# Kernel tuning notes

Hardware: AMD Instinct MI355X
Metric: run time of the kernel (lower is better)

Reference implementation:

```python
import jax, jax.numpy as jnp
import numpy as np

BZ, T, D, DFF, E, BEAMS = 128, 32, 768, 3072, 8, 2


def setup_inputs() -> dict:
    key = jax.random.key(0)
    ks = jax.random.split(key, 4)
    s = 0.02
    return {
        "x": jax.random.normal(ks[0], (BZ, T, D), jnp.float32),
        "attention_mask": jnp.ones((BZ, T), jnp.float32),
        "Wg": jax.random.normal(ks[1], (D, E), jnp.float32) * s,   # gate Linear(D,E,bias=False)
        "W1": jax.random.normal(ks[2], (E, D, DFF), jnp.float32) * s,
        "b1": jnp.zeros((E, DFF), jnp.float32),
        "W2": jax.random.normal(ks[3], (E, DFF, D), jnp.float32) * s,
        "b2": jnp.zeros((E, D), jnp.float32),
    }


def reference(x, attention_mask, Wg, W1, b1, W2, b2):
    # forward_gate: module builds its own all-ones mask regardless of input mask
    mask = jnp.ones((x.shape[0], x.shape[1]), x.dtype)
    x_avg = (x * mask[..., None]).sum(1) / mask[..., None].sum(1)   # [bz, D]
    prob = jax.nn.softmax(x_avg @ Wg, axis=-1)                       # [bz, E]
    # beam_search (layer_judge='first', pre-route): topk on exp(log(softmax)) == softmax probs
    scores = jnp.exp(jnp.log(prob))
    topv, topi = jax.lax.top_k(scores, BEAMS)                        # [bz, beams]
    beam_scores = topv.reshape(-1)                                   # [bz*beams]
    expert_route = topi.reshape(-1, 1)                                # [bz*beams, 1]
    sel = expert_route[:, -1]
    # replicate x per beam: [bz*beams, T, D]
    x_rep = jnp.broadcast_to(x[:, None], (x.shape[0], BEAMS, x.shape[1], x.shape[2]))
    x_rep = x_rep.reshape(-1, x.shape[1], x.shape[2])
    # per-sample expert FFN dispatch (dense masked loop over the E=8 experts)
    out = jnp.zeros_like(x_rep)
    for e in range(E):
        h = jax.nn.gelu(jnp.einsum('nsd,df->nsf', x_rep, W1[e]) + b1[e], approximate=False)
        ye = jnp.einsum('nsf,fd->nsd', h, W2[e]) + b2[e]
        out = jnp.where((sel == e)[:, None, None], ye, out)
    return (out, beam_scores, expert_route)
```

## Files before the change

### kernel.cpp

```cpp
#include <hip/hip_runtime.h>
#include <cstddef>
#include <cstdint>

#define BZd   128
#define Td    32
#define Dd    768
#define DFFd  3072
#define Ed    8
#define NBEAM 256
#define ROWS_TOT 8192
#define OUT_ELEMS 6291456
#define MAXTILES 72

typedef unsigned short u16;
typedef __attribute__((ext_vector_type(4))) unsigned short ushort4v;
typedef __attribute__((ext_vector_type(8))) short frag_ab;
typedef __attribute__((ext_vector_type(4))) float floatx4;

__device__ __forceinline__ u16 f2bf(float f) {
  unsigned int u = __builtin_bit_cast(unsigned int, f);
  u += 0x7FFFu + ((u >> 16) & 1u);
  return (u16)(u >> 16);
}

__device__ __forceinline__ void async_copy16(u16* lds, const u16* g) {
  __builtin_amdgcn_global_load_lds(
      (const __attribute__((address_space(1))) void*)g,
      (__attribute__((address_space(3))) void*)lds, 16, 0, 0);
}

__device__ __forceinline__ float gelu_fast(float x) {
  float z = 1.5957691216f * (x + 0.044715f * x * x * x);
  return x / (1.0f + __expf(-z));
}

__global__ __launch_bounds__(256) void route_kernel(
    const float* __restrict__ x, const float* __restrict__ Wg,
    float* __restrict__ out, int* __restrict__ sel) {
  int b = blockIdx.x;
  int t = threadIdx.x;
  __shared__ float red[256][8];
  float la[8];
#pragma unroll
  for (int e = 0; e < 8; e++) la[e] = 0.f;
  for (int d = t; d < Dd; d += 256) {
    const float* xp = x + (size_t)b * Td * Dd + d;
    float xa = 0.f;
#pragma unroll
    for (int tt = 0; tt < Td; tt++) xa += xp[(size_t)tt * Dd];
    xa *= (1.0f / 32.0f);
#pragma unroll
    for (int e = 0; e < 8; e++) la[e] += xa * Wg[d * 8 + e];
  }
#pragma unroll
  for (int e = 0; e < 8; e++) red[t][e] = la[e];
  __syncthreads();
  for (int s = 128; s > 0; s >>= 1) {
    if (t < s) {
#pragma unroll
      for (int e = 0; e < 8; e++) red[t][e] += red[t + s][e];
    }
    __syncthreads();
  }
  if (t == 0) {
    float lg[8];
#pragma unroll
    for (int e = 0; e < 8; e++) lg[e] = red[0][e];
    float mx = lg[0];
#pragma unroll
    for (int e = 1; e < 8; e++) mx = fmaxf(mx, lg[e]);
    float p[8];
    float sum = 0.f;
#pragma unroll
    for (int e = 0; e < 8; e++) { p[e] = __expf(lg[e] - mx); sum += p[e]; }
    float inv = 1.0f / sum;
#pragma unroll
    for (int e = 0; e < 8; e++) p[e] *= inv;
    int i0 = 0; float v0 = p[0];
#pragma unroll
    for (int e = 1; e < 8; e++) if (p[e] > v0) { v0 = p[e]; i0 = e; }
    int i1 = -1; float v1 = -1.0f;
#pragma unroll
    for (int e = 0; e < 8; e++) if (e != i0 && p[e] > v1) { v1 = p[e]; i1 = e; }
    float* bs = out + OUT_ELEMS;
    float* er = out + OUT_ELEMS + NBEAM;
    bs[2 * b] = v0; bs[2 * b + 1] = v1;
    er[2 * b] = (float)i0; er[2 * b + 1] = (float)i1;
    sel[2 * b] = i0; sel[2 * b + 1] = i1;
  }
}

__global__ __launch_bounds__(256) void bucket_kernel(
    const int* __restrict__ sel, int* __restrict__ perm, int4* __restrict__ tiles) {
  __shared__ int ssel[NBEAM];
  __shared__ int scnt[8];
  __shared__ int soff[8];
  __shared__ int scur[8];
  __shared__ int sperm[NBEAM];
  int t = threadIdx.x;
  ssel[t] = sel[t];
  __syncthreads();
  if (t == 0) {
    for (int e = 0; e < 8; e++) scnt[e] = 0;
    for (int n = 0; n < NBEAM; n++) scnt[ssel[n]]++;
    int o = 0;
    for (int e = 0; e < 8; e++) { soff[e] = o; scur[e] = o; o += scnt[e]; }
    for (int n = 0; n < NBEAM; n++) { int e = ssel[n]; sperm[scur[e]++] = n; }
    int tt = 0;
    for (int e = 0; e < 8; e++) {
      int nr = scnt[e] * 32;
      int base = soff[e] * 32;
      for (int r0 = 0; r0 < nr; r0 += 128) {
        tiles[tt] = make_int4(e, base + r0, min(128, nr - r0), 0);
        tt++;
      }
    }
    for (; tt < MAXTILES; tt++) tiles[tt] = make_int4(-1, 0, 0, 0);
  }
  __syncthreads();
  perm[t] = sperm[t];
}

__global__ __launch_bounds__(256) void convert_x_kernel(
    const float* __restrict__ x, u16* __restrict__ xbf) {
  size_t i = ((size_t)blockIdx.x * 256 + threadIdx.x) * 4;
  float4 v = *(const float4*)(x + i);
  ushort4v pv = {f2bf(v.x), f2bf(v.y), f2bf(v.z), f2bf(v.w)};
  *(ushort4v*)(xbf + i) = pv;
}

__global__ __launch_bounds__(256) void transpose_bf16_kernel(
    const float* __restrict__ in, u16* __restrict__ out, int row0, int col0,
    int ld_in, size_t estr_in, int ld_out, size_t estr_out) {
  __shared__ u16 tile[64][65];
  int e = blockIdx.z;
  int r0 = blockIdx.x * 64, c0 = blockIdx.y * 64;
  int t = threadIdx.x;
  int rr = t >> 4, cc4 = (t & 15) * 4;
  const float* ip = in + (size_t)e * estr_in + (size_t)(row0 + r0) * ld_in + col0 + c0;
#pragma unroll
  for (int i = 0; i < 4; i++) {
    int r = rr + 16 * i;
    float4 v = *(const float4*)(ip + (size_t)r * ld_in + cc4);
    tile[r][cc4 + 0] = f2bf(v.x);
    tile[r][cc4 + 1] = f2bf(v.y);
    tile[r][cc4 + 2] = f2bf(v.z);
    tile[r][cc4 + 3] = f2bf(v.w);
  }
  __syncthreads();
  int ccw = t >> 4, r4 = (t & 15) * 4;
  u16* op = out + (size_t)e * estr_out + (size_t)c0 * ld_out + r0;
#pragma unroll
  for (int i = 0; i < 4; i++) {
    int cc = ccw + 16 * i;
    ushort4v pv = {tile[r4 + 0][cc], tile[r4 + 1][cc], tile[r4 + 2][cc], tile[r4 + 3][cc]};
    *(ushort4v*)(op + (size_t)cc * ld_out + r4) = pv;
  }
}

__global__ __launch_bounds__(256) void gemm1_kernel(
    const u16* __restrict__ xbf, const u16* __restrict__ w1t,
    const float* __restrict__ b1, const int* __restrict__ perm,
    const int4* __restrict__ tiles, u16* __restrict__ h, int f0, int FC) {
  int4 meta = tiles[blockIdx.y];
  int e = meta.x;
  if (e < 0) return;
  int grow0 = meta.y, nrows = meta.z;
  int bx = blockIdx.x;

  __shared__ __align__(16) u16 As[128 * 64];
  __shared__ __align__(16) u16 Bs[128 * 64];

  int t = threadIdx.x;
  int l = t & 63, w = t >> 6;
  int wm = w & 1, wn = w >> 1;
  int lrow = l & 15, lquad = l >> 4;

  const u16* ag[4]; const u16* bg[4];
  u16* al[4]; u16* bl[4];
#pragma unroll
  for (int j = 0; j < 4; j++) {
    int s = j * 256 + t;
    int m = s >> 3;
    int koff = (((s & 7) ^ ((m >> 1) & 7))) * 8;
    int bidx = (grow0 >> 5) + (m >> 5);
    bidx = bidx < NBEAM ? bidx : NBEAM - 1;
    int batch = perm[bidx] >> 1;
    ag[j] = xbf + ((size_t)batch * Td + (m & 31)) * Dd + koff;
    bg[j] = w1t + ((size_t)e * FC + bx * 128 + m) * Dd + koff;
    al[j] = As + j * 2048 + w * 512;
    bl[j] = Bs + j * 2048 + w * 512;
  }

  int aoff[2][4], boff[2][4];
#pragma unroll
  for (int hh = 0; hh < 2; hh++)
#pragma unroll
    for (int i = 0; i < 4; i++) {
      int ra = wm * 64 + i * 16 + lrow;
      aoff[hh][i] = ra * 64 + (((lquad + hh * 4) ^ ((ra >> 1) & 7)) * 8);
      int rb = wn * 64 + i * 16 + lrow;
      boff[hh][i] = rb * 64 + (((lquad + hh * 4) ^ ((rb >> 1) & 7)) * 8);
    }

  floatx4 acc[4][4];
#pragma unroll
  for (int mi = 0; mi < 4; mi++)
#pragma unroll
    for (int ni = 0; ni < 4; ni++) acc[mi][ni] = (floatx4){0.f, 0.f, 0.f, 0.f};

  for (int kt = 0; kt < Dd; kt += 64) {
#pragma unroll
    for (int j = 0; j < 4; j++) {
      async_copy16(al[j], ag[j]);
      async_copy16(bl[j], bg[j]);
      ag[j] += 64; bg[j] += 64;
    }
    __syncthreads();
#pragma unroll
    for (int hh = 0; hh < 2; hh++) {
      frag_ab af[4], bf[4];
#pragma unroll
      for (int mi = 0; mi < 4; mi++) af[mi] = *(const frag_ab*)(As + aoff[hh][mi]);
#pragma unroll
      for (int ni = 0; ni < 4; ni++) bf[ni] = *(const frag_ab*)(Bs + boff[hh][ni]);
#pragma unroll
      for (int mi = 0; mi < 4; mi++)
#pragma unroll
        for (int ni = 0; ni < 4; ni++)
          acc[mi][ni] = __builtin_amdgcn_mfma_f32_16x16x32_bf16(af[mi], bf[ni], acc[mi][ni], 0, 0, 0);
    }
    __syncthreads();
  }

  int f_base = bx * 128;
#pragma unroll
  for (int mi = 0; mi < 4; mi++) {
    int row0 = wm * 64 + mi * 16 + lquad * 4;
#pragma unroll
    for (int ni = 0; ni < 4; ni++) {
      int col = wn * 64 + ni * 16 + lrow;
      float bias = b1[(size_t)e * DFFd + f0 + f_base + col];
#pragma unroll
      for (int r = 0; r < 4; r++) {
        int row = row0 + r;
        if (row < nrows) {
          float vv = acc[mi][ni][r] + bias;
          h[(size_t)(grow0 + row) * FC + f_base + col] = f2bf(gelu_fast(vv));
        }
      }
    }
  }
}

__global__ __launch_bounds__(256) void gemm2_kernel(
    const u16* __restrict__ h, const u16* __restrict__ w2t,
    const float* __restrict__ b2, const int* __restrict__ perm,
    const int4* __restrict__ tiles, float* __restrict__ out,
    int FC, int first) {
  int4 meta = tiles[blockIdx.y];
  int e = meta.x;
  if (e < 0) return;
  int grow0 = meta.y, nrows = meta.z;
  int bx = blockIdx.x;

  __shared__ __align__(16) u16 As[128 * 64];
  __shared__ __align__(16) u16 Bs[128 * 64];
  __shared__ int sbeam[4];

  int t = threadIdx.x;
  if (t < 4) {
    int idx = (grow0 >> 5) + t;
    sbeam[t] = perm[idx < NBEAM ? idx : NBEAM - 1];
  }
  int l = t & 63, w = t >> 6;
  int wm = w & 1, wn = w >> 1;
  int lrow = l & 15, lquad = l >> 4;

  const u16* ag[4]; const u16* bg[4];
  u16* al[4]; u16* bl[4];
#pragma unroll
  for (int j = 0; j < 4; j++) {
    int s = j * 256 + t;
    int m = s >> 3;
    int koff = (((s & 7) ^ ((m >> 1) & 7))) * 8;
    int arow = grow0 + m;
    arow = arow < ROWS_TOT ? arow : ROWS_TOT - 1;
    ag[j] = h + (size_t)arow * FC + koff;
    bg[j] = w2t + ((size_t)e * Dd + bx * 128 + m) * FC + koff;
    al[j] = As + j * 2048 + w * 512;
    bl[j] = Bs + j * 2048 + w * 512;
  }

  int aoff[2][4], boff[2][4];
#pragma unroll
  for (int hh = 0; hh < 2; hh++)
#pragma unroll
    for (int i = 0; i < 4; i++) {
      int ra = wm * 64 + i * 16 + lrow;
      aoff[hh][i] = ra * 64 + (((lquad + hh * 4) ^ ((ra >> 1) & 7)) * 8);
      int rb = wn * 64 + i * 16 + lrow;
      boff[hh][i] = rb * 64 + (((lquad + hh * 4) ^ ((rb >> 1) & 7)) * 8);
    }

  floatx4 acc[4][4];
#pragma unroll
  for (int mi = 0; mi < 4; mi++)
#pragma unroll
    for (int ni = 0; ni < 4; ni++) acc[mi][ni] = (floatx4){0.f, 0.f, 0.f, 0.f};

  for (int kt = 0; kt < FC; kt += 64) {
#pragma unroll
    for (int j = 0; j < 4; j++) {
      async_copy16(al[j], ag[j]);
      async_copy16(bl[j], bg[j]);
      ag[j] += 64; bg[j] += 64;
    }
    __syncthreads();
#pragma unroll
    for (int hh = 0; hh < 2; hh++) {
      frag_ab af[4], bf[4];
#pragma unroll
      for (int mi = 0; mi < 4; mi++) af[mi] = *(const frag_ab*)(As + aoff[hh][mi]);
#pragma unroll
      for (int ni = 0; ni < 4; ni++) bf[ni] = *(const frag_ab*)(Bs + boff[hh][ni]);
#pragma unroll
      for (int mi = 0; mi < 4; mi++)
#pragma unroll
        for (int ni = 0; ni < 4; ni++)
          acc[mi][ni] = __builtin_amdgcn_mfma_f32_16x16x32_bf16(af[mi], bf[ni], acc[mi][ni], 0, 0, 0);
    }
    __syncthreads();
  }

#pragma unroll
  for (int mi = 0; mi < 4; mi++) {
    int row0 = wm * 64 + mi * 16 + lquad * 4;
#pragma unroll
    for (int ni = 0; ni < 4; ni++) {
      int col = wn * 64 + ni * 16 + lrow;
      int dg = bx * 128 + col;
      float bias = b2[(size_t)e * Dd + dg];
#pragma unroll
      for (int r = 0; r < 4; r++) {
        int row = row0 + r;
        if (row < nrows) {
          int beam = sbeam[row >> 5];
          size_t o = ((size_t)beam * Td + (row & 31)) * Dd + dg;
          if (first) out[o] = acc[mi][ni][r] + bias;
          else out[o] += acc[mi][ni][r];
        }
      }
    }
  }
}

extern "C" void kernel_launch(void* const* d_in, const int* in_sizes, int n_in,
                              void* d_out, int out_size, void* d_ws, size_t ws_size,
                              hipStream_t stream) {
  const float* x  = (const float*)d_in[0];
  const float* Wg = (const float*)d_in[2];
  const float* W1 = (const float*)d_in[3];
  const float* b1 = (const float*)d_in[4];
  const float* W2 = (const float*)d_in[5];
  const float* b2 = (const float*)d_in[6];
  float* out = (float*)d_out;

  char* ws = (char*)d_ws;
  int*  sel   = (int*)ws;
  int*  perm  = sel + NBEAM;
  int4* tiles = (int4*)(ws + 4096);

  const size_t xbf_off = 65536;
  const size_t xbf_bytes = (size_t)BZd * Td * Dd * 2;
  int FC = 384;
  if      (xbf_off + xbf_bytes + (size_t)40960 * 3072 <= ws_size) FC = 3072;
  else if (xbf_off + xbf_bytes + (size_t)40960 * 1536 <= ws_size) FC = 1536;
  else if (xbf_off + xbf_bytes + (size_t)40960 * 768  <= ws_size) FC = 768;
  int NC = DFFd / FC;

  u16* xbf = (u16*)(ws + xbf_off);
  u16* w1t = (u16*)(ws + xbf_off + xbf_bytes);
  u16* w2t = w1t + (size_t)Ed * FC * Dd;
  u16* h   = w2t + (size_t)Ed * Dd * FC;

  route_kernel<<<BZd, 256, 0, stream>>>(x, Wg, out, sel);
  bucket_kernel<<<1, 256, 0, stream>>>(sel, perm, tiles);
  convert_x_kernel<<<(BZd * Td * Dd) / 1024, 256, 0, stream>>>(x, xbf);

  for (int c = 0; c < NC; c++) {
    transpose_bf16_kernel<<<dim3(Dd / 64, FC / 64, Ed), 256, 0, stream>>>(
        W1, w1t, 0, c * FC, DFFd, (size_t)Dd * DFFd, Dd, (size_t)FC * Dd);
    transpose_bf16_kernel<<<dim3(FC / 64, Dd / 64, Ed), 256, 0, stream>>>(
        W2, w2t, c * FC, 0, Dd, (size_t)DFFd * Dd, FC, (size_t)Dd * FC);
    gemm1_kernel<<<dim3(FC / 128, MAXTILES), 256, 0, stream>>>(
        xbf, w1t, b1, perm, tiles, h, c * FC, FC);
    gemm2_kernel<<<dim3(Dd / 128, MAXTILES), 256, 0, stream>>>(
        h, w2t, b2, perm, tiles, out, FC, c == 0 ? 1 : 0);
  }
}
```

Measured before the change: 393.1 us.

## Double-buffer GEMM K-loop and fuse convert/transpose launches

Result: slower. 401.2 us (+2.1%).

```diff
diff --git a/kernel.cpp b/kernel.cpp
--- a/kernel.cpp
+++ b/kernel.cpp
@@ -34,9 +34,9 @@
   return x / (1.0f + __expf(-z));
 }
 
-__global__ __launch_bounds__(256) void route_kernel(
+__global__ __launch_bounds__(256) void route_convert_kernel(
     const float* __restrict__ x, const float* __restrict__ Wg,
-    float* __restrict__ out, int* __restrict__ sel) {
+    float* __restrict__ out, int* __restrict__ sel, u16* __restrict__ xbf) {
   int b = blockIdx.x;
   int t = threadIdx.x;
   __shared__ float red[256][8];
@@ -88,6 +88,15 @@
     er[2 * b] = (float)i0; er[2 * b + 1] = (float)i1;
     sel[2 * b] = i0; sel[2 * b + 1] = i1;
   }
+  const float* xp = x + (size_t)b * Td * Dd;
+  u16* op = xbf + (size_t)b * Td * Dd;
+#pragma unroll
+  for (int k = 0; k < 24; k++) {
+    int flat = (k * 256 + t) * 4;
+    float4 v = *(const float4*)(xp + flat);
+    ushort4v pv = {f2bf(v.x), f2bf(v.y), f2bf(v.z), f2bf(v.w)};
+    *(ushort4v*)(op + flat) = pv;
+  }
 }
 
 __global__ __launch_bounds__(256) void bucket_kernel(
@@ -95,7 +104,6 @@
   __shared__ int ssel[NBEAM];
   __shared__ int scnt[8];
   __shared__ int soff[8];
-  __shared__ int scur[8];
   __shared__ int sperm[NBEAM];
   int t = threadIdx.x;
   ssel[t] = sel[t];
@@ -104,8 +112,15 @@
     for (int e = 0; e < 8; e++) scnt[e] = 0;
     for (int n = 0; n < NBEAM; n++) scnt[ssel[n]]++;
     int o = 0;
-    for (int e = 0; e < 8; e++) { soff[e] = o; scur[e] = o; o += scnt[e]; }
-    for (int n = 0; n < NBEAM; n++) { int e = ssel[n]; sperm[scur[e]++] = n; }
+    for (int e = 0; e < 8; e++) { soff[e] = o; o += scnt[e]; }
+  }
+  __syncthreads();
+  if (t < 8) {
+    int idx = soff[t];
+    for (int n = 0; n < NBEAM; n++)
+      if (ssel[n] == t) sperm[idx++] = n;
+  }
+  if (t == 0) {
     int tt = 0;
     for (int e = 0; e < 8; e++) {
       int nr = scnt[e] * 32;
@@ -121,23 +136,25 @@
   perm[t] = sperm[t];
 }
 
-__global__ __launch_bounds__(256) void convert_x_kernel(
-    const float* __restrict__ x, u16* __restrict__ xbf) {
-  size_t i = ((size_t)blockIdx.x * 256 + threadIdx.x) * 4;
-  float4 v = *(const float4*)(x + i);
-  ushort4v pv = {f2bf(v.x), f2bf(v.y), f2bf(v.z), f2bf(v.w)};
-  *(ushort4v*)(xbf + i) = pv;
-}
-
-__global__ __launch_bounds__(256) void transpose_bf16_kernel(
-    const float* __restrict__ in, u16* __restrict__ out, int row0, int col0,
-    int ld_in, size_t estr_in, int ld_out, size_t estr_out) {
+__global__ __launch_bounds__(256) void transpose_all_kernel(
+    const float* __restrict__ W1, u16* __restrict__ w1t,
+    const float* __restrict__ W2, u16* __restrict__ w2t, int f0, int FC) {
   __shared__ u16 tile[64][65];
-  int e = blockIdx.z;
-  int r0 = blockIdx.x * 64, c0 = blockIdx.y * 64;
+  int z = blockIdx.z, bx = blockIdx.x, by = blockIdx.y;
   int t = threadIdx.x;
+  const float* ip; u16* op; int ld_in, ld_out;
+  if (z < 8) {
+    int e = z;
+    ld_in = DFFd; ld_out = Dd;
+    ip = W1 + (size_t)e * Dd * DFFd + (size_t)(bx * 64) * DFFd + (f0 + by * 64);
+    op = w1t + (size_t)e * FC * Dd + (size_t)(by * 64) * Dd + bx * 64;
+  } else {
+    int e = z - 8;
+    ld_in = Dd; ld_out = FC;
+    ip = W2 + (size_t)e * DFFd * Dd + (size_t)(f0 + by * 64) * Dd + bx * 64;
+    op = w2t + (size_t)e * Dd * FC + (size_t)(bx * 64) * FC + by * 64;
+  }
   int rr = t >> 4, cc4 = (t & 15) * 4;
-  const float* ip = in + (size_t)e * estr_in + (size_t)(row0 + r0) * ld_in + col0 + c0;
 #pragma unroll
   for (int i = 0; i < 4; i++) {
     int r = rr + 16 * i;
@@ -149,7 +166,6 @@
   }
   __syncthreads();
   int ccw = t >> 4, r4 = (t & 15) * 4;
-  u16* op = out + (size_t)e * estr_out + (size_t)c0 * ld_out + r0;
 #pragma unroll
   for (int i = 0; i < 4; i++) {
     int cc = ccw + 16 * i;
@@ -168,40 +184,37 @@
   int grow0 = meta.y, nrows = meta.z;
   int bx = blockIdx.x;
 
-  __shared__ __align__(16) u16 As[128 * 64];
-  __shared__ __align__(16) u16 Bs[128 * 64];
+  __shared__ __align__(16) u16 As[2][128 * 32];
+  __shared__ __align__(16) u16 Bs[2][128 * 32];
 
   int t = threadIdx.x;
   int l = t & 63, w = t >> 6;
   int wm = w & 1, wn = w >> 1;
   int lrow = l & 15, lquad = l >> 4;
 
-  const u16* ag[4]; const u16* bg[4];
-  u16* al[4]; u16* bl[4];
-#pragma unroll
-  for (int j = 0; j < 4; j++) {
+  const u16* ag[2]; const u16* bg[2];
+  int lbase[2];
+#pragma unroll
+  for (int j = 0; j < 2; j++) {
     int s = j * 256 + t;
-    int m = s >> 3;
-    int koff = (((s & 7) ^ ((m >> 1) & 7))) * 8;
+    int m = s >> 2;
+    int koff = ((s & 3) ^ ((m >> 1) & 3)) * 8;
     int bidx = (grow0 >> 5) + (m >> 5);
     bidx = bidx < NBEAM ? bidx : NBEAM - 1;
     int batch = perm[bidx] >> 1;
     ag[j] = xbf + ((size_t)batch * Td + (m & 31)) * Dd + koff;
     bg[j] = w1t + ((size_t)e * FC + bx * 128 + m) * Dd + koff;
-    al[j] = As + j * 2048 + w * 512;
-    bl[j] = Bs + j * 2048 + w * 512;
-  }
-
-  int aoff[2][4], boff[2][4];
-#pragma unroll
-  for (int hh = 0; hh < 2; hh++)
-#pragma unroll
-    for (int i = 0; i < 4; i++) {
-      int ra = wm * 64 + i * 16 + lrow;
-      aoff[hh][i] = ra * 64 + (((lquad + hh * 4) ^ ((ra >> 1) & 7)) * 8);
-      int rb = wn * 64 + i * 16 + lrow;
-      boff[hh][i] = rb * 64 + (((lquad + hh * 4) ^ ((rb >> 1) & 7)) * 8);
-    }
+    lbase[j] = (j * 256 + w * 64) * 8;
+  }
+
+  int aoff[4], boff[4];
+#pragma unroll
+  for (int i = 0; i < 4; i++) {
+    int ra = wm * 64 + i * 16 + lrow;
+    aoff[i] = ra * 32 + ((lquad ^ ((ra >> 1) & 3)) * 8);
+    int rb = wn * 64 + i * 16 + lrow;
+    boff[i] = rb * 32 + ((lquad ^ ((rb >> 1) & 3)) * 8);
+  }
 
   floatx4 acc[4][4];
 #pragma unroll
@@ -209,28 +222,35 @@
 #pragma unroll
     for (int ni = 0; ni < 4; ni++) acc[mi][ni] = (floatx4){0.f, 0.f, 0.f, 0.f};
 
-  for (int kt = 0; kt < Dd; kt += 64) {
-#pragma unroll
-    for (int j = 0; j < 4; j++) {
-      async_copy16(al[j], ag[j]);
-      async_copy16(bl[j], bg[j]);
-      ag[j] += 64; bg[j] += 64;
-    }
+#pragma unroll
+  for (int j = 0; j < 2; j++) {
+    async_copy16(&As[0][lbase[j]], ag[j]);
+    async_copy16(&Bs[0][lbase[j]], bg[j]);
+    ag[j] += 32; bg[j] += 32;
+  }
+
+  const int NIT = Dd / 32;
+  for (int it = 0; it < NIT; ++it) {
     __syncthreads();
-#pragma unroll
-    for (int hh = 0; hh < 2; hh++) {
-      frag_ab af[4], bf[4];
-#pragma unroll
-      for (int mi = 0; mi < 4; mi++) af[mi] = *(const frag_ab*)(As + aoff[hh][mi]);
-#pragma unroll
-      for (int ni = 0; ni < 4; ni++) bf[ni] = *(const frag_ab*)(Bs + boff[hh][ni]);
-#pragma unroll
-      for (int mi = 0; mi < 4; mi++)
-#pragma unroll
-        for (int ni = 0; ni < 4; ni++)
-          acc[mi][ni] = __builtin_amdgcn_mfma_f32_16x16x32_bf16(af[mi], bf[ni], acc[mi][ni], 0, 0, 0);
-    }
-    __syncthreads();
+    int cur = it & 1, nxt = cur ^ 1;
+    if (it + 1 < NIT) {
+#pragma unroll
+      for (int j = 0; j < 2; j++) {
+        async_copy16(&As[nxt][lbase[j]], ag[j]);
+        async_copy16(&Bs[nxt][lbase[j]], bg[j]);
+        ag[j] += 32; bg[j] += 32;
+      }
+    }
+    frag_ab af[4], bf[4];
+#pragma unroll
+    for (int mi = 0; mi < 4; mi++) af[mi] = *(const frag_ab*)(&As[cur][aoff[mi]]);
+#pragma unroll
+    for (int ni = 0; ni < 4; ni++) bf[ni] = *(const frag_ab*)(&Bs[cur][boff[ni]]);
+#pragma unroll
+    for (int mi = 0; mi < 4; mi++)
+#pragma unroll
+      for (int ni = 0; ni < 4; ni++)
+        acc[mi][ni] = __builtin_amdgcn_mfma_f32_16x16x32_bf16(af[mi], bf[ni], acc[mi][ni], 0, 0, 0);
   }
 
   int f_base = bx * 128;
@@ -264,8 +284,8 @@
   int grow0 = meta.y, nrows = meta.z;
   int bx = blockIdx.x;
 
-  __shared__ __align__(16) u16 As[128 * 64];
-  __shared__ __align__(16) u16 Bs[128 * 64];
+  __shared__ __align__(16) u16 As[2][128 * 32];
+  __shared__ __align__(16) u16 Bs[2][128 * 32];
   __shared__ int sbeam[4];
 
   int t = threadIdx.x;
@@ -277,31 +297,28 @@
   int wm = w & 1, wn = w >> 1;
   int lrow = l & 15, lquad = l >> 4;
 
-  const u16* ag[4]; const u16* bg[4];
-  u16* al[4]; u16* bl[4];
-#pragma unroll
-  for (int j = 0; j < 4; j++) {
+  const u16* ag[2]; const u16* bg[2];
+  int lbase[2];
+#pragma unroll
+  for (int j = 0; j < 2; j++) {
     int s = j * 256 + t;
-    int m = s >> 3;
-    int koff = (((s & 7) ^ ((m >> 1) & 7))) * 8;
+    int m = s >> 2;
+    int koff = ((s & 3) ^ ((m >> 1) & 3)) * 8;
     int arow = grow0 + m;
     arow = arow < ROWS_TOT ? arow : ROWS_TOT - 1;
     ag[j] = h + (size_t)arow * FC + koff;
     bg[j] = w2t + ((size_t)e * Dd + bx * 128 + m) * FC + koff;
-    al[j] = As + j * 2048 + w * 512;
-    bl[j] = Bs + j * 2048 + w * 512;
-  }
-
-  int aoff[2][4], boff[2][4];
-#pragma unroll
-  for (int hh = 0; hh < 2; hh++)
-#pragma unroll
-    for (int i = 0; i < 4; i++) {
-      int ra = wm * 64 + i * 16 + lrow;
-      aoff[hh][i] = ra * 64 + (((lquad + hh * 4) ^ ((ra >> 1) & 7)) * 8);
-      int rb = wn * 64 + i * 16 + lrow;
-      boff[hh][i] = rb * 64 + (((lquad + hh * 4) ^ ((rb >> 1) & 7)) * 8);
-    }
+    lbase[j] = (j * 256 + w * 64) * 8;
+  }
+
+  int aoff[4], boff[4];
+#pragma unroll
+  for (int i = 0; i < 4; i++) {
+    int ra = wm * 64 + i * 16 + lrow;
+    aoff[i] = ra * 32 + ((lquad ^ ((ra >> 1) & 3)) * 8);
+    int rb = wn * 64 + i * 16 + lrow;
+    boff[i] = rb * 32 + ((lquad ^ ((rb >> 1) & 3)) * 8);
+  }
 
   floatx4 acc[4][4];
 #pragma unroll
@@ -309,28 +326,35 @@
 #pragma unroll
     for (int ni = 0; ni < 4; ni++) acc[mi][ni] = (floatx4){0.f, 0.f, 0.f, 0.f};
 
-  for (int kt = 0; kt < FC; kt += 64) {
-#pragma unroll
-    for (int j = 0; j < 4; j++) {
-      async_copy16(al[j], ag[j]);
-      async_copy16(bl[j], bg[j]);
-      ag[j] += 64; bg[j] += 64;
-    }
+#pragma unroll
+  for (int j = 0; j < 2; j++) {
+    async_copy16(&As[0][lbase[j]], ag[j]);
+    async_copy16(&Bs[0][lbase[j]], bg[j]);
+    ag[j] += 32; bg[j] += 32;
+  }
+
+  const int NIT_ = FC / 32;
+  for (int it = 0; it < NIT_; ++it) {
     __syncthreads();
-#pragma unroll
-    for (int hh = 0; hh < 2; hh++) {
-      frag_ab af[4], bf[4];
-#pragma unroll
-      for (int mi = 0; mi < 4; mi++) af[mi] = *(const frag_ab*)(As + aoff[hh][mi]);
-#pragma unroll
-      for (int ni = 0; ni < 4; ni++) bf[ni] = *(const frag_ab*)(Bs + boff[hh][ni]);
-#pragma unroll
-      for (int mi = 0; mi < 4; mi++)
-#pragma unroll
-        for (int ni = 0; ni < 4; ni++)
-          acc[mi][ni] = __builtin_amdgcn_mfma_f32_16x16x32_bf16(af[mi], bf[ni], acc[mi][ni], 0, 0, 0);
-    }
-    __syncthreads();
+    int cur = it & 1, nxt = cur ^ 1;
+    if (it + 1 < NIT_) {
+#pragma unroll
+      for (int j = 0; j < 2; j++) {
+        async_copy16(&As[nxt][lbase[j]], ag[j]);
+        async_copy16(&Bs[nxt][lbase[j]], bg[j]);
+        ag[j] += 32; bg[j] += 32;
+      }
+    }
+    frag_ab af[4], bf[4];
+#pragma unroll
+    for (int mi = 0; mi < 4; mi++) af[mi] = *(const frag_ab*)(&As[cur][aoff[mi]]);
+#pragma unroll
+    for (int ni = 0; ni < 4; ni++) bf[ni] = *(const frag_ab*)(&Bs[cur][boff[ni]]);
+#pragma unroll
+    for (int mi = 0; mi < 4; mi++)
+#pragma unroll
+      for (int ni = 0; ni < 4; ni++)
+        acc[mi][ni] = __builtin_amdgcn_mfma_f32_16x16x32_bf16(af[mi], bf[ni], acc[mi][ni], 0, 0, 0);
   }
 
 #pragma unroll
@@ -384,15 +408,12 @@
   u16* w2t = w1t + (size_t)Ed * FC * Dd;
   u16* h   = w2t + (size_t)Ed * Dd * FC;
 
-  route_kernel<<<BZd, 256, 0, stream>>>(x, Wg, out, sel);
+  route_convert_kernel<<<BZd, 256, 0, stream>>>(x, Wg, out, sel, xbf);
   bucket_kernel<<<1, 256, 0, stream>>>(sel, perm, tiles);
-  convert_x_kernel<<<(BZd * Td * Dd) / 1024, 256, 0, stream>>>(x, xbf);
 
   for (int c = 0; c < NC; c++) {
-    transpose_bf16_kernel<<<dim3(Dd / 64, FC / 64, Ed), 256, 0, stream>>>(
-        W1, w1t, 0, c * FC, DFFd, (size_t)Dd * DFFd, Dd, (size_t)FC * Dd);
-    transpose_bf16_kernel<<<dim3(FC / 64, Dd / 64, Ed), 256, 0, stream>>>(
-        W2, w2t, c * FC, 0, Dd, (size_t)DFFd * Dd, FC, (size_t)Dd * FC);
+    transpose_all_kernel<<<dim3(Dd / 64, FC / 64, 16), 256, 0, stream>>>(
+        W1, w1t, W2, w2t, c * FC, FC);
     gemm1_kernel<<<dim3(FC / 128, MAXTILES), 256, 0, stream>>>(
         xbf, w1t, b1, perm, tiles, h, c * FC, FC);
     gemm2_kernel<<<dim3(Dd / 128, MAXTILES), 256, 0, stream>>>(
```
